# Optimization experiments

Measured on AMD Instinct MI355X. Metric: run time of the kernel, lower is better.

Reference implementation:

```python
import jax, jax.numpy as jnp
import numpy as np

EPS = 1e-5
NUM_MEM_TOKENS = 16
SEGMENT_SIZE = 512


def dpfp(x):
    # DPFP feature map (Schlag et al.), nu=1: doubles the last dim, all-nonnegative.
    x2 = jnp.concatenate([jax.nn.relu(x), jax.nn.relu(-x)], axis=-1)
    return x2 * jnp.roll(x2, 1, axis=-1)


def setup_inputs() -> dict:
    key = jax.random.key(0)
    ks = jax.random.split(key, 7)
    B, S, D, DM = 4, 4224, 1024, 64  # S = n_seg * (segment_size + num_mem_tokens) = 8*528
    scale = 0.02
    return {
        "hidden_states": jax.random.normal(ks[0], (B, S, D), jnp.float32),
        "model_output": jax.random.normal(ks[1], (B, S, D), jnp.float32),
        "W_mq": jax.random.normal(ks[2], (D, DM), jnp.float32) * scale,
        "W_mk": jax.random.normal(ks[3], (D, DM), jnp.float32) * scale,
        "W_mv": jax.random.normal(ks[4], (D, D), jnp.float32) * scale,
        "W_mb": jax.random.normal(ks[5], (D, D), jnp.float32) * scale,
        "b_mb": jnp.zeros((D,), jnp.float32),
    }


def reference(hidden_states, model_output, W_mq, W_mk, W_mv, W_mb, b_mb):
    B, S, D = hidden_states.shape
    L = SEGMENT_SIZE + NUM_MEM_TOKENS
    n_seg = S // L
    d_key = 2 * W_mq.shape[1]  # dpfp doubles feature dim

    # [n_seg, B, L, D]
    h = hidden_states.reshape(B, n_seg, L, D).transpose(1, 0, 2, 3)
    m = model_output.reshape(B, n_seg, L, D).transpose(1, 0, 2, 3)

    def step(carry, seg):
        W_mem, z = carry  # [B, d_key, D], [B, d_key]
        hid, mo = seg     # [B, L, D] each
        # --- associate: linear-attention read of compressive memory ---
        q = dpfp(hid @ W_mq)                                   # [B, L, d_key]
        num = jnp.einsum('blk,bkd->bld', q, W_mem)             # [B, L, D]
        den = jnp.einsum('blk,bk->bl', q, z)[..., None] + EPS
        assoc = num / den
        # --- delta-rule memory update from memory tokens of segment output ---
        mem = (assoc + mo)[:, -NUM_MEM_TOKENS:]                # [B, M, D]
        k = dpfp(mem @ W_mk)                                   # [B, M, d_key]
        v = mem @ W_mv                                         # [B, M, D]
        gate = jax.nn.sigmoid(mem @ W_mb + b_mb)               # [B, M, D]
        prev = jnp.einsum('bmk,bkd->bmd', k, W_mem) / (
            jnp.einsum('bmk,bk->bm', k, z)[..., None] + EPS)   # correction (old value)
        new_info = gate * (v - prev)
        W_mem = W_mem + jnp.einsum('bmk,bmd->bkd', k, new_info)
        z = z + k.sum(axis=1)
        return (W_mem, z), assoc

    W0 = jnp.zeros((B, d_key, D), hidden_states.dtype)
    z0 = jnp.zeros((B, d_key), hidden_states.dtype)
    _, assocs = jax.lax.scan(step, (W0, z0), (h, m))           # [n_seg, B, L, D]
    association = jnp.tanh(assocs.transpose(1, 0, 2, 3).reshape(B, S, D))
    return model_output + association
```

## Files before the change

kernel.cpp:

```cpp
#include <hip/hip_runtime.h>
#include <hip/hip_bf16.h>

#define EPS 1e-5f

typedef short s8v __attribute__((ext_vector_type(8)));
typedef float f4v __attribute__((ext_vector_type(4)));

__device__ __forceinline__ unsigned short f2bf(float f) {
  unsigned u = __builtin_bit_cast(unsigned, f);
  u = u + 0x7FFFu + ((u >> 16) & 1u);
  return (unsigned short)(u >> 16);
}
__device__ __forceinline__ float bf2f(unsigned short h) {
  unsigned u = ((unsigned)h) << 16;
  return __builtin_bit_cast(float, u);
}
__device__ __forceinline__ float fast_tanh(float x) {
  float e = __expf(2.0f * x);
  return 1.0f - 2.0f / (e + 1.0f);
}
__device__ __forceinline__ float fast_sigmoid(float x) {
  return 1.0f / (1.0f + __expf(-x));
}
__device__ __forceinline__ float frcp(float x) { return __builtin_amdgcn_rcpf(x); }

__global__ __launch_bounds__(256) void transpose_kernel(
    const float* __restrict__ W_mq, const float* __restrict__ W_mk,
    const float* __restrict__ W_mv, const float* __restrict__ W_mb,
    unsigned short* __restrict__ W_mqT, unsigned short* __restrict__ W_mkT,
    unsigned short* __restrict__ W_mvT, unsigned short* __restrict__ W_mbT) {
  __shared__ float tile[32][33];
  int bid = blockIdx.x;
  const float* src; unsigned short* dst; int N, t0;
  if (bid < 64)        { src = W_mq; dst = W_mqT; N = 64;   t0 = bid; }
  else if (bid < 128)  { src = W_mk; dst = W_mkT; N = 64;   t0 = bid - 64; }
  else if (bid < 1152) { src = W_mv; dst = W_mvT; N = 1024; t0 = bid - 128; }
  else                 { src = W_mb; dst = W_mbT; N = 1024; t0 = bid - 1152; }
  const int K = 1024;
  int tk = t0 & 31, tn = t0 >> 5;
  int k0 = tk * 32, n0 = tn * 32;
  int t = threadIdx.x;
  int cr = t >> 5, cc = t & 31;
#pragma unroll
  for (int u = 0; u < 4; u++) {
    int row = cr + u * 8;
    tile[row][cc] = src[(size_t)(k0 + row) * N + n0 + cc];
  }
  __syncthreads();
#pragma unroll
  for (int u = 0; u < 4; u++) {
    int nl = cr + u * 8;
    dst[(size_t)(n0 + nl) * K + k0 + cc] = f2bf(tile[cc][nl]);
  }
}

union QLdsU { float y[16 * 64]; unsigned short kq[16 * 128]; };

__device__ void q_tile_pair(const float* __restrict__ HS,
                            const unsigned short* __restrict__ W_mqT,
                            unsigned short* __restrict__ Q, int tile,
                            char* qsmem) {
  QLdsU* lds = (QLdsU*)qsmem;
  int t = threadIdx.x & 127, wv = t >> 6, lane = t & 63, m = lane & 15, q = lane >> 4;
  int r0 = tile * 16;
  const float* ap = HS + (size_t)(r0 + m) * 1024 + wv * 512 + q * 8;
  const unsigned short* bp = W_mqT + (size_t)m * 1024 + wv * 512 + q * 8;
  f4v acc[4] = {f4v{0,0,0,0}, f4v{0,0,0,0}, f4v{0,0,0,0}, f4v{0,0,0,0}};
#pragma unroll 4
  for (int ks = 0; ks < 16; ks++) {
    int k0 = ks * 32;
    f4v h0 = *(const f4v*)(ap + k0);
    f4v h1 = *(const f4v*)(ap + k0 + 4);
    s8v a;
    a[0] = (short)f2bf(h0[0]); a[1] = (short)f2bf(h0[1]);
    a[2] = (short)f2bf(h0[2]); a[3] = (short)f2bf(h0[3]);
    a[4] = (short)f2bf(h1[0]); a[5] = (short)f2bf(h1[1]);
    a[6] = (short)f2bf(h1[2]); a[7] = (short)f2bf(h1[3]);
#pragma unroll
    for (int nf = 0; nf < 4; nf++) {
      s8v b = *(const s8v*)(bp + nf * 16384 + k0);
      acc[nf] = __builtin_amdgcn_mfma_f32_16x16x32_bf16(a, b, acc[nf], 0, 0, 0);
    }
  }
  if (wv == 1) {
#pragma unroll
    for (int nf = 0; nf < 4; nf++)
#pragma unroll
      for (int i = 0; i < 4; i++)
        lds->y[(nf * 4 + i) * 64 + lane] = acc[nf][i];
  }
  __syncthreads();
  if (wv == 0) {
#pragma unroll
    for (int nf = 0; nf < 4; nf++)
#pragma unroll
      for (int i = 0; i < 4; i++)
        acc[nf][i] += lds->y[(nf * 4 + i) * 64 + lane];
    int srcl = (lane & 48) | ((m + 15) & 15);
#pragma unroll
    for (int i = 0; i < 4; i++) {
      float yp[4];
#pragma unroll
      for (int nf = 0; nf < 4; nf++) yp[nf] = __shfl(acc[nf][i], srcl);
      int r = q * 4 + i;
#pragma unroll
      for (int nf = 0; nf < 4; nf++) {
        float yv = acc[nf][i];
        float py = (m != 0) ? yp[nf] : (nf > 0 ? yp[nf - 1] : yp[3]);
        bool wrap = (m == 0 && nf == 0);
        float x2lo = wrap ? fmaxf(-py, 0.f) : fmaxf(py, 0.f);
        float x2hi = wrap ? fmaxf(py, 0.f) : fmaxf(-py, 0.f);
        lds->kq[r * 128 + nf * 16 + m]      = f2bf(fmaxf(yv, 0.f) * x2lo);
        lds->kq[r * 128 + 64 + nf * 16 + m] = f2bf(fmaxf(-yv, 0.f) * x2hi);
      }
    }
  }
  __syncthreads();
  {
    int row = t >> 3, ch = t & 7;
    unsigned short* qp = Q + (size_t)(r0 + row) * 128 + ch * 16;
    *(s8v*)(qp)     = *(const s8v*)&lds->kq[row * 128 + ch * 16];
    *(s8v*)(qp + 8) = *(const s8v*)&lds->kq[row * 128 + ch * 16 + 8];
  }
}

__device__ void scan_role(
    const float* __restrict__ HS, const unsigned short* __restrict__ W_mqT,
    const unsigned short* __restrict__ Qb, const unsigned short* __restrict__ W_mkT,
    const unsigned short* __restrict__ W_mvT, const unsigned short* __restrict__ W_mbT,
    const float* __restrict__ b_mb, const float* __restrict__ MO,
    float* __restrict__ OUT, unsigned short* __restrict__ hist,
    float* __restrict__ zh, unsigned short* __restrict__ mem_bf,
    int* bar, int* qflags, char* smem) {
  float* Wf           = (float*)smem;
  unsigned short* Wbf = (unsigned short*)(smem + 32768);
  float* y_lds        = (float*)(smem + 49664);
  float* k_f          = (float*)(smem + 53760);
  unsigned short* k_bf= (unsigned short*)(smem + 61952);
  float* kden_l       = (float*)(smem + 66304);
  float* ni_lds       = (float*)(smem + 66368);
  float* z_l          = (float*)(smem + 70528);

  int t = threadIdx.x, wv = t >> 6, lane = t & 63, m = lane & 15, q = lane >> 4;
  int ct = blockIdx.x & 15, b = blockIdx.x >> 4;
  int col = ct * 64 + wv * 16 + m;

  if (blockIdx.x < 16) {
    int pair = t >> 7;
    int sp = blockIdx.x * 2 + pair;
    int tile = (sp >> 3) * 264 + (sp & 7) * 33 + 32;
    q_tile_pair(HS, W_mqT, (unsigned short*)Qb, tile, smem + pair * 4096);
    __syncthreads();
    if (t == 0) { __threadfence(); atomicAdd(qflags, 2); }
  }

  for (int i = t; i < 128 * 64; i += 256) Wf[i] = 0.f;
  for (int i = t; i < 64 * 132; i += 256) Wbf[i] = 0;
  if (t < 128) z_l[t] = 0.f;
  float bmb = b_mb[col];
  if (t == 0) {
    while (__hip_atomic_load(qflags, __ATOMIC_RELAXED, __HIP_MEMORY_SCOPE_AGENT) < 32)
      __builtin_amdgcn_s_sleep(1);
    __threadfence();
  }
  __syncthreads();

  s8v aq[4]; float mo_pf[4];
  {
    const unsigned short* qp = Qb + ((size_t)b * 4224 + 512 + m) * 128;
#pragma unroll
    for (int ks = 0; ks < 4; ks++) aq[ks] = *(const s8v*)(qp + ks * 32 + q * 8);
    const float* mop = MO + ((size_t)b * 4224 + 512 + q * 4) * 1024 + col;
#pragma unroll
    for (int i = 0; i < 4; i++) mo_pf[i] = mop[(size_t)i * 1024];
  }

  for (int s = 0; s < 8; s++) {
    {
      float dp = 0.f;
#pragma unroll
      for (int ks = 0; ks < 4; ks++)
#pragma unroll
        for (int j = 0; j < 8; j++)
          dp += bf2f((unsigned short)aq[ks][j]) * z_l[ks * 32 + q * 8 + j];
      dp += __shfl_xor(dp, 16);
      dp += __shfl_xor(dp, 32);
      dp += EPS;
      f4v acc = {0, 0, 0, 0};
#pragma unroll
      for (int ks = 0; ks < 4; ks++) {
        s8v bv = *(const s8v*)&Wbf[(wv * 16 + m) * 132 + ks * 32 + q * 8];
        acc = __builtin_amdgcn_mfma_f32_16x16x32_bf16(aq[ks], bv, acc, 0, 0, 0);
      }
      unsigned short* mb = mem_bf + (s & 1) * 65536 + b * 16384;
      size_t grow = (size_t)b * 4224 + s * 528 + 512;
#pragma unroll
      for (int i = 0; i < 4; i++) {
        float rden = frcp(__shfl(dp, q * 4 + i));
        float assoc = acc[i] * rden;
        float mov = mo_pf[i];
        OUT[(grow + q * 4 + i) * 1024 + col] = mov + fast_tanh(assoc);
        mb[(q * 4 + i) * 1024 + col] = f2bf(assoc + mov);
      }
    }
    __syncthreads();
    if (t == 0) {
      __threadfence();
      atomicAdd(bar + s * 4 + b, 1);
      while (__hip_atomic_load(bar + s * 4 + b, __ATOMIC_RELAXED,
                               __HIP_MEMORY_SCOPE_AGENT) < 16)
        __builtin_amdgcn_s_sleep(1);
      __threadfence();
    }
    __syncthreads();
    f4v accv = {0,0,0,0}, accg = {0,0,0,0};
    {
      const unsigned short* avp = mem_bf + (s & 1) * 65536 + b * 16384 + m * 1024 + q * 8;
      const unsigned short* bkp = W_mkT + (size_t)(wv * 16 + m) * 1024 + q * 8;
      const unsigned short* bvp = W_mvT + (size_t)col * 1024 + q * 8;
      const unsigned short* bgp = W_mbT + (size_t)col * 1024 + q * 8;
      f4v acy = {0, 0, 0, 0};
#pragma unroll 4
      for (int ks = 0; ks < 32; ks++) {
        s8v av = *(const s8v*)(avp + ks * 32);
        s8v bk = *(const s8v*)(bkp + ks * 32);
        s8v bv = *(const s8v*)(bvp + ks * 32);
        s8v bg = *(const s8v*)(bgp + ks * 32);
        acy  = __builtin_amdgcn_mfma_f32_16x16x32_bf16(av, bk, acy, 0, 0, 0);
        accv = __builtin_amdgcn_mfma_f32_16x16x32_bf16(av, bv, accv, 0, 0, 0);
        accg = __builtin_amdgcn_mfma_f32_16x16x32_bf16(av, bg, accg, 0, 0, 0);
      }
#pragma unroll
      for (int i = 0; i < 4; i++) y_lds[(q * 4 + i) * 64 + wv * 16 + m] = acy[i];
    }
    __syncthreads();
    {
      int r = t >> 4, jg = t & 15;
      const float* yr = &y_lds[r * 64];
      float pd = 0.f;
#pragma unroll
      for (int u = 0; u < 8; u++) {
        int jj = jg * 8 + u, jm = (jj + 127) & 127;
        float yj = (jj < 64) ? yr[jj] : -yr[jj - 64];
        float ym = (jm < 64) ? yr[jm] : -yr[jm - 64];
        float kv = fmaxf(yj, 0.f) * fmaxf(ym, 0.f);
        k_f[r * 128 + jj] = kv;
        k_bf[r * 136 + jj] = f2bf(kv);
        pd += kv * z_l[jj];
      }
      pd += __shfl_xor(pd, 1);
      pd += __shfl_xor(pd, 2);
      pd += __shfl_xor(pd, 4);
      pd += __shfl_xor(pd, 8);
      if (jg == 0) kden_l[r] = pd + EPS;
    }
    __syncthreads();
    {
      f4v accp = {0, 0, 0, 0};
#pragma unroll
      for (int ks = 0; ks < 4; ks++) {
        s8v ak = *(const s8v*)&k_bf[m * 136 + ks * 32 + q * 8];
        s8v bm = *(const s8v*)&Wbf[(wv * 16 + m) * 132 + ks * 32 + q * 8];
        accp = __builtin_amdgcn_mfma_f32_16x16x32_bf16(ak, bm, accp, 0, 0, 0);
      }
#pragma unroll
      for (int i = 0; i < 4; i++) {
        int r = q * 4 + i;
        float prev = accp[i] * frcp(kden_l[r]);
        float g = fast_sigmoid(accg[i] + bmb);
        ni_lds[r * 65 + wv * 16 + m] = g * (accv[i] - prev);
      }
      if (t < 128) {
        float ssum = 0.f;
#pragma unroll
        for (int r = 0; r < 16; r++) ssum += k_f[r * 128 + t];
        z_l[t] += ssum;
        if (s < 7) zh[(s + 1) * 512 + b * 128 + t] = z_l[t];
      }
    }
    __syncthreads();
    {
      int cl = t & 63, kg = t >> 6;
      float niv[16];
#pragma unroll
      for (int mm = 0; mm < 16; mm++) niv[mm] = ni_lds[mm * 65 + cl];
      float delta[32];
#pragma unroll
      for (int jj = 0; jj < 32; jj++) delta[jj] = 0.f;
#pragma unroll
      for (int mm = 0; mm < 16; mm++) {
        const float* kb = &k_f[mm * 128 + kg * 32];
        float nv = niv[mm];
#pragma unroll
        for (int ch = 0; ch < 8; ch++) {
          f4v kv4 = *(const f4v*)(kb + ch * 4);
#pragma unroll
          for (int jj = 0; jj < 4; jj++) delta[ch * 4 + jj] += kv4[jj] * nv;
        }
      }
      unsigned short* hdst = hist + (size_t)(s + 1) * 524288 +
                             ((size_t)b * 1024 + ct * 64 + cl) * 128 + kg * 32;
#pragma unroll
      for (int c8 = 0; c8 < 4; c8++) {
        s8v pk;
#pragma unroll
        for (int u = 0; u < 8; u++) {
          int kk = kg * 32 + c8 * 8 + u;
          float nv = Wf[kk * 64 + cl] + delta[c8 * 8 + u];
          Wf[kk * 64 + cl] = nv;
          pk[u] = (short)f2bf(nv);
        }
        *(s8v*)&Wbf[cl * 132 + kg * 32 + c8 * 8] = pk;
        if (s < 7) *(s8v*)(hdst + c8 * 8) = pk;
      }
      if (s < 7) {
        const unsigned short* qp = Qb + ((size_t)b * 4224 + (s + 1) * 528 + 512 + m) * 128;
#pragma unroll
        for (int ks = 0; ks < 4; ks++) aq[ks] = *(const s8v*)(qp + ks * 32 + q * 8);
        const float* mop = MO + ((size_t)b * 4224 + (s + 1) * 528 + 512 + q * 4) * 1024 + col;
#pragma unroll
        for (int i = 0; i < 4; i++) mo_pf[i] = mop[(size_t)i * 1024];
      }
    }
    __syncthreads();
  }
}

__device__ void worker_role(
    const float* __restrict__ HS, const unsigned short* __restrict__ W_mqT,
    unsigned short* __restrict__ Qb, const unsigned short* __restrict__ hist,
    const float* __restrict__ zh, const float* __restrict__ MO,
    float* __restrict__ OUT, int* bar, int* qflags, char* smem) {
  int w = (int)blockIdx.x - 64;
  int t = threadIdx.x;
  int pair = t >> 7;
  int np = 0;
  for (int p = w; p < 512; p += 192) {
    int rr = 2 * p + pair;
    int tile = (rr >> 8) * 264 + ((rr & 255) >> 5) * 33 + (rr & 31);
    q_tile_pair(HS, W_mqT, Qb, tile, smem + pair * 4096);
    np++;
    __syncthreads();
  }
  if (t == 0) { __threadfence(); atomicAdd(qflags + 1, np); }
  for (int idx = w; idx < 512; idx += 192) {
    int b = idx & 3, ct = (idx >> 2) & 15, rt4 = idx >> 6;
    int r = t >> 2, cchunk = (t & 3) * 16;
    size_t rbase = ((size_t)b * 4224 + (size_t)rt4 * 64 + r) * 1024 + ct * 64 + cchunk;
#pragma unroll
    for (int u = 0; u < 4; u++)
      *(f4v*)(OUT + rbase + u * 4) = *(const f4v*)(MO + rbase + u * 4);
  }
  if (t == 0) {
    while (__hip_atomic_load(qflags + 1, __ATOMIC_RELAXED, __HIP_MEMORY_SCOPE_AGENT) < 512)
      __builtin_amdgcn_s_sleep(1);
    __threadfence();
  }
  __syncthreads();
  int wv = t >> 6, lane = t & 63, m = lane & 15, q = lane >> 4;
  float* as_l = (float*)smem;
  for (int idx = 512 + w; idx < 4096; idx += 192) {
    int seg = idx >> 9, inner = idx & 511;
    int b = inner & 3, ct = (inner >> 2) & 15, rt4 = inner >> 6;
    if (t == 0) {
      while (__hip_atomic_load(bar + seg * 4 + b, __ATOMIC_RELAXED,
                               __HIP_MEMORY_SCOPE_AGENT) < 16)
        __builtin_amdgcn_s_sleep(2);
      __threadfence();
    }
    __syncthreads();
    const unsigned short* Wm = hist + (size_t)seg * 524288 + ((size_t)b * 1024 + ct * 64) * 128;
    const float* zp = zh + seg * 512 + b * 128;
    size_t grow = (size_t)b * 4224 + (size_t)seg * 528 + rt4 * 64 + wv * 16;
    const unsigned short* qp = Qb + (grow + m) * 128;
    s8v a[4];
    float dp = 0.f;
#pragma unroll
    for (int ks = 0; ks < 4; ks++) {
      a[ks] = *(const s8v*)(qp + ks * 32 + q * 8);
      f4v z0 = *(const f4v*)(zp + ks * 32 + q * 8);
      f4v z1 = *(const f4v*)(zp + ks * 32 + q * 8 + 4);
#pragma unroll
      for (int j = 0; j < 4; j++) dp += bf2f((unsigned short)a[ks][j]) * z0[j];
#pragma unroll
      for (int j = 0; j < 4; j++) dp += bf2f((unsigned short)a[ks][j + 4]) * z1[j];
    }
    dp += __shfl_xor(dp, 16);
    dp += __shfl_xor(dp, 32);
    dp += EPS;
    f4v acc[4] = {f4v{0,0,0,0}, f4v{0,0,0,0}, f4v{0,0,0,0}, f4v{0,0,0,0}};
#pragma unroll
    for (int ks = 0; ks < 4; ks++) {
#pragma unroll
      for (int nf = 0; nf < 4; nf++) {
        s8v bv = *(const s8v*)(Wm + (size_t)(nf * 16 + m) * 128 + ks * 32 + q * 8);
        acc[nf] = __builtin_amdgcn_mfma_f32_16x16x32_bf16(a[ks], bv, acc[nf], 0, 0, 0);
      }
    }
#pragma unroll
    for (int i = 0; i < 4; i++) {
      float rden = frcp(__shfl(dp, q * 4 + i));
#pragma unroll
      for (int nf = 0; nf < 4; nf++)
        as_l[(wv * 16 + q * 4 + i) * 65 + nf * 16 + m] = acc[nf][i] * rden;
    }
    __syncthreads();
    {
      int r = t >> 2, cchunk = (t & 3) * 16;
      size_t rbase = (grow - wv * 16 + r) * 1024 + ct * 64 + cchunk;
      const float* ar = &as_l[r * 65 + cchunk];
#pragma unroll
      for (int u = 0; u < 4; u++) {
        f4v mo = *(const f4v*)(MO + rbase + u * 4);
        f4v o;
#pragma unroll
        for (int j = 0; j < 4; j++) o[j] = mo[j] + fast_tanh(ar[u * 4 + j]);
        *(f4v*)(OUT + rbase + u * 4) = o;
      }
    }
    __syncthreads();
  }
}

__global__ __launch_bounds__(256, 1) void fused_kernel(
    const float* __restrict__ HS, const unsigned short* __restrict__ W_mqT,
    const unsigned short* __restrict__ W_mkT, const unsigned short* __restrict__ W_mvT,
    const unsigned short* __restrict__ W_mbT, const float* __restrict__ b_mb,
    const float* __restrict__ MO, float* __restrict__ OUT,
    unsigned short* __restrict__ Qb, unsigned short* __restrict__ hist,
    float* __restrict__ zh, unsigned short* __restrict__ mem_bf,
    int* bar, int* qflags) {
  __shared__ __align__(16) char smem[71040];
  if (blockIdx.x < 64) {
    scan_role(HS, W_mqT, Qb, W_mkT, W_mvT, W_mbT, b_mb, MO, OUT,
              hist, zh, mem_bf, bar, qflags, smem);
  } else {
    worker_role(HS, W_mqT, Qb, hist, zh, MO, OUT, bar, qflags, smem);
  }
}

extern "C" void kernel_launch(void* const* d_in, const int* in_sizes, int n_in,
                              void* d_out, int out_size, void* d_ws, size_t ws_size,
                              hipStream_t stream) {
  const float* HS  = (const float*)d_in[0];
  const float* MO  = (const float*)d_in[1];
  const float* W_mq = (const float*)d_in[2];
  const float* W_mk = (const float*)d_in[3];
  const float* W_mv = (const float*)d_in[4];
  const float* W_mb = (const float*)d_in[5];
  const float* b_mb = (const float*)d_in[6];
  float* OUT = (float*)d_out;

  char* wsb = (char*)d_ws;
  unsigned short* hist   = (unsigned short*)(wsb + 0);
  float*          zh     = (float*)(wsb + 8388608);
  unsigned short* Qb     = (unsigned short*)(wsb + 8404992);
  unsigned short* W_mqT  = (unsigned short*)(wsb + 12730368);
  unsigned short* W_mkT  = (unsigned short*)(wsb + 12861440);
  unsigned short* W_mvT  = (unsigned short*)(wsb + 12992512);
  unsigned short* W_mbT  = (unsigned short*)(wsb + 15089664);
  unsigned short* mem_bf = (unsigned short*)(wsb + 17186816);
  int*            bar    = (int*)(wsb + 17448960);
  int*            qflags = (int*)(wsb + 0);

  (void)hipMemsetAsync(wsb, 0, 256, stream);
  (void)hipMemsetAsync(bar, 0, 128, stream);
  transpose_kernel<<<2176, 256, 0, stream>>>(W_mq, W_mk, W_mv, W_mb,
                                             W_mqT, W_mkT, W_mvT, W_mbT);
  fused_kernel<<<256, 256, 0, stream>>>(HS, W_mqT, W_mkT, W_mvT, W_mbT, b_mb,
                                        MO, OUT, Qb, hist, zh, mem_bf, bar, qflags);
}
```

Before: 527.9 us.

## Use atomic work queue for bulk tiles, double grid, pad barrier counters

Bulk output tiles are now pulled from a global atomic work queue instead of a static stride, and scan blocks join the bulk loop once their sequential scan finishes. The grid doubles to 512 blocks with launch bounds allowing 2 blocks per CU, and per-segment barrier counters are padded to separate cache lines with longer sleep intervals. The goal is better load balance and more latency hiding across the bulk phase. In exchange, scan blocks may now share CUs with worker blocks and slow the serial critical path, and the spin barriers rely on all 512 blocks being co-resident.

New measurement: 787.7 us. +49.2%, slower.

```diff
diff --git a/kernel.cpp b/kernel.cpp
--- a/kernel.cpp
+++ b/kernel.cpp
@@ -124,6 +124,80 @@
   }
 }
 
+__device__ void bulk_loop(const unsigned short* __restrict__ Qb,
+                          const unsigned short* __restrict__ hist,
+                          const float* __restrict__ zh,
+                          const float* __restrict__ MO, float* __restrict__ OUT,
+                          int* bar, int* wq, char* smem) {
+  int t = threadIdx.x, wv = t >> 6, lane = t & 63, m = lane & 15, q = lane >> 4;
+  float* as_l = (float*)smem;
+  int* sidx = (int*)(smem + 16640);
+  for (;;) {
+    if (t == 0) sidx[0] = atomicAdd(wq, 1);
+    __syncthreads();
+    int idx = sidx[0] + 512;
+    if (idx >= 4096) break;
+    int seg = idx >> 9, inner = idx & 511;
+    int b = inner & 3, ct = (inner >> 2) & 15, rt4 = inner >> 6;
+    if (t == 0) {
+      while (__hip_atomic_load(bar + (seg * 4 + b) * 16, __ATOMIC_RELAXED,
+                               __HIP_MEMORY_SCOPE_AGENT) < 16)
+        __builtin_amdgcn_s_sleep(8);
+      __threadfence();
+    }
+    __syncthreads();
+    const unsigned short* Wm = hist + (size_t)seg * 524288 + ((size_t)b * 1024 + ct * 64) * 128;
+    const float* zp = zh + seg * 512 + b * 128;
+    size_t grow = (size_t)b * 4224 + (size_t)seg * 528 + rt4 * 64 + wv * 16;
+    const unsigned short* qp = Qb + (grow + m) * 128;
+    s8v a[4];
+    float dp = 0.f;
+#pragma unroll
+    for (int ks = 0; ks < 4; ks++) {
+      a[ks] = *(const s8v*)(qp + ks * 32 + q * 8);
+      f4v z0 = *(const f4v*)(zp + ks * 32 + q * 8);
+      f4v z1 = *(const f4v*)(zp + ks * 32 + q * 8 + 4);
+#pragma unroll
+      for (int j = 0; j < 4; j++) dp += bf2f((unsigned short)a[ks][j]) * z0[j];
+#pragma unroll
+      for (int j = 0; j < 4; j++) dp += bf2f((unsigned short)a[ks][j + 4]) * z1[j];
+    }
+    dp += __shfl_xor(dp, 16);
+    dp += __shfl_xor(dp, 32);
+    dp += EPS;
+    f4v acc[4] = {f4v{0,0,0,0}, f4v{0,0,0,0}, f4v{0,0,0,0}, f4v{0,0,0,0}};
+#pragma unroll
+    for (int ks = 0; ks < 4; ks++) {
+#pragma unroll
+      for (int nf = 0; nf < 4; nf++) {
+        s8v bv = *(const s8v*)(Wm + (size_t)(nf * 16 + m) * 128 + ks * 32 + q * 8);
+        acc[nf] = __builtin_amdgcn_mfma_f32_16x16x32_bf16(a[ks], bv, acc[nf], 0, 0, 0);
+      }
+    }
+#pragma unroll
+    for (int i = 0; i < 4; i++) {
+      float rden = frcp(__shfl(dp, q * 4 + i));
+#pragma unroll
+      for (int nf = 0; nf < 4; nf++)
+        as_l[(wv * 16 + q * 4 + i) * 65 + nf * 16 + m] = acc[nf][i] * rden;
+    }
+    __syncthreads();
+    {
+      int r = t >> 2, cchunk = (t & 3) * 16;
+      size_t rbase = (grow - wv * 16 + r) * 1024 + ct * 64 + cchunk;
+      const float* ar = &as_l[r * 65 + cchunk];
+#pragma unroll
+      for (int u = 0; u < 4; u++) {
+        f4v mo = *(const f4v*)(MO + rbase + u * 4);
+        f4v o;
+#pragma unroll
+        for (int j = 0; j < 4; j++) o[j] = mo[j] + fast_tanh(ar[u * 4 + j]);
+        *(f4v*)(OUT + rbase + u * 4) = o;
+      }
+    }
+  }
+}
+
 __device__ void scan_role(
     const float* __restrict__ HS, const unsigned short* __restrict__ W_mqT,
     const unsigned short* __restrict__ Qb, const unsigned short* __restrict__ W_mkT,
@@ -131,7 +205,7 @@
     const float* __restrict__ b_mb, const float* __restrict__ MO,
     float* __restrict__ OUT, unsigned short* __restrict__ hist,
     float* __restrict__ zh, unsigned short* __restrict__ mem_bf,
-    int* bar, int* qflags, char* smem) {
+    int* bar, int* qflags, int* wq, char* smem) {
   float* Wf           = (float*)smem;
   unsigned short* Wbf = (unsigned short*)(smem + 32768);
   float* y_lds        = (float*)(smem + 49664);
@@ -206,8 +280,8 @@
     __syncthreads();
     if (t == 0) {
       __threadfence();
-      atomicAdd(bar + s * 4 + b, 1);
-      while (__hip_atomic_load(bar + s * 4 + b, __ATOMIC_RELAXED,
+      atomicAdd(bar + (s * 4 + b) * 16, 1);
+      while (__hip_atomic_load(bar + (s * 4 + b) * 16, __ATOMIC_RELAXED,
                                __HIP_MEMORY_SCOPE_AGENT) < 16)
         __builtin_amdgcn_s_sleep(1);
       __threadfence();
@@ -324,18 +398,27 @@
     }
     __syncthreads();
   }
+
+  if (t == 0) {
+    while (__hip_atomic_load(qflags + 1, __ATOMIC_RELAXED, __HIP_MEMORY_SCOPE_AGENT) < 512)
+      __builtin_amdgcn_s_sleep(8);
+    __threadfence();
+  }
+  __syncthreads();
+  bulk_loop(Qb, hist, zh, MO, OUT, bar, wq, smem);
 }
 
 __device__ void worker_role(
     const float* __restrict__ HS, const unsigned short* __restrict__ W_mqT,
     unsigned short* __restrict__ Qb, const unsigned short* __restrict__ hist,
     const float* __restrict__ zh, const float* __restrict__ MO,
-    float* __restrict__ OUT, int* bar, int* qflags, char* smem) {
+    float* __restrict__ OUT, int* bar, int* qflags, int* wq, char* smem) {
+  int nw = (int)gridDim.x - 64;
   int w = (int)blockIdx.x - 64;
   int t = threadIdx.x;
   int pair = t >> 7;
   int np = 0;
-  for (int p = w; p < 512; p += 192) {
+  for (int p = w; p < 512; p += nw) {
     int rr = 2 * p + pair;
     int tile = (rr >> 8) * 264 + ((rr & 255) >> 5) * 33 + (rr & 31);
     q_tile_pair(HS, W_mqT, Qb, tile, smem + pair * 4096);
@@ -343,7 +426,7 @@
     __syncthreads();
   }
   if (t == 0) { __threadfence(); atomicAdd(qflags + 1, np); }
-  for (int idx = w; idx < 512; idx += 192) {
+  for (int idx = w; idx < 512; idx += nw) {
     int b = idx & 3, ct = (idx >> 2) & 15, rt4 = idx >> 6;
     int r = t >> 2, cchunk = (t & 3) * 16;
     size_t rbase = ((size_t)b * 4224 + (size_t)rt4 * 64 + r) * 1024 + ct * 64 + cchunk;
@@ -353,89 +436,27 @@
   }
   if (t == 0) {
     while (__hip_atomic_load(qflags + 1, __ATOMIC_RELAXED, __HIP_MEMORY_SCOPE_AGENT) < 512)
-      __builtin_amdgcn_s_sleep(1);
+      __builtin_amdgcn_s_sleep(8);
     __threadfence();
   }
   __syncthreads();
-  int wv = t >> 6, lane = t & 63, m = lane & 15, q = lane >> 4;
-  float* as_l = (float*)smem;
-  for (int idx = 512 + w; idx < 4096; idx += 192) {
-    int seg = idx >> 9, inner = idx & 511;
-    int b = inner & 3, ct = (inner >> 2) & 15, rt4 = inner >> 6;
-    if (t == 0) {
-      while (__hip_atomic_load(bar + seg * 4 + b, __ATOMIC_RELAXED,
-                               __HIP_MEMORY_SCOPE_AGENT) < 16)
-        __builtin_amdgcn_s_sleep(2);
-      __threadfence();
-    }
-    __syncthreads();
-    const unsigned short* Wm = hist + (size_t)seg * 524288 + ((size_t)b * 1024 + ct * 64) * 128;
-    const float* zp = zh + seg * 512 + b * 128;
-    size_t grow = (size_t)b * 4224 + (size_t)seg * 528 + rt4 * 64 + wv * 16;
-    const unsigned short* qp = Qb + (grow + m) * 128;
-    s8v a[4];
-    float dp = 0.f;
-#pragma unroll
-    for (int ks = 0; ks < 4; ks++) {
-      a[ks] = *(const s8v*)(qp + ks * 32 + q * 8);
-      f4v z0 = *(const f4v*)(zp + ks * 32 + q * 8);
-      f4v z1 = *(const f4v*)(zp + ks * 32 + q * 8 + 4);
-#pragma unroll
-      for (int j = 0; j < 4; j++) dp += bf2f((unsigned short)a[ks][j]) * z0[j];
-#pragma unroll
-      for (int j = 0; j < 4; j++) dp += bf2f((unsigned short)a[ks][j + 4]) * z1[j];
-    }
-    dp += __shfl_xor(dp, 16);
-    dp += __shfl_xor(dp, 32);
-    dp += EPS;
-    f4v acc[4] = {f4v{0,0,0,0}, f4v{0,0,0,0}, f4v{0,0,0,0}, f4v{0,0,0,0}};
-#pragma unroll
-    for (int ks = 0; ks < 4; ks++) {
-#pragma unroll
-      for (int nf = 0; nf < 4; nf++) {
-        s8v bv = *(const s8v*)(Wm + (size_t)(nf * 16 + m) * 128 + ks * 32 + q * 8);
-        acc[nf] = __builtin_amdgcn_mfma_f32_16x16x32_bf16(a[ks], bv, acc[nf], 0, 0, 0);
-      }
-    }
-#pragma unroll
-    for (int i = 0; i < 4; i++) {
-      float rden = frcp(__shfl(dp, q * 4 + i));
-#pragma unroll
-      for (int nf = 0; nf < 4; nf++)
-        as_l[(wv * 16 + q * 4 + i) * 65 + nf * 16 + m] = acc[nf][i] * rden;
-    }
-    __syncthreads();
-    {
-      int r = t >> 2, cchunk = (t & 3) * 16;
-      size_t rbase = (grow - wv * 16 + r) * 1024 + ct * 64 + cchunk;
-      const float* ar = &as_l[r * 65 + cchunk];
-#pragma unroll
-      for (int u = 0; u < 4; u++) {
-        f4v mo = *(const f4v*)(MO + rbase + u * 4);
-        f4v o;
-#pragma unroll
-        for (int j = 0; j < 4; j++) o[j] = mo[j] + fast_tanh(ar[u * 4 + j]);
-        *(f4v*)(OUT + rbase + u * 4) = o;
-      }
-    }
-    __syncthreads();
-  }
-}
-
-__global__ __launch_bounds__(256, 1) void fused_kernel(
+  bulk_loop(Qb, hist, zh, MO, OUT, bar, wq, smem);
+}
+
+__global__ __launch_bounds__(256, 2) void fused_kernel(
     const float* __restrict__ HS, const unsigned short* __restrict__ W_mqT,
     const unsigned short* __restrict__ W_mkT, const unsigned short* __restrict__ W_mvT,
     const unsigned short* __restrict__ W_mbT, const float* __restrict__ b_mb,
     const float* __restrict__ MO, float* __restrict__ OUT,
     unsigned short* __restrict__ Qb, unsigned short* __restrict__ hist,
     float* __restrict__ zh, unsigned short* __restrict__ mem_bf,
-    int* bar, int* qflags) {
+    int* bar, int* qflags, int* wq) {
   __shared__ __align__(16) char smem[71040];
   if (blockIdx.x < 64) {
     scan_role(HS, W_mqT, Qb, W_mkT, W_mvT, W_mbT, b_mb, MO, OUT,
-              hist, zh, mem_bf, bar, qflags, smem);
+              hist, zh, mem_bf, bar, qflags, wq, smem);
   } else {
-    worker_role(HS, W_mqT, Qb, hist, zh, MO, OUT, bar, qflags, smem);
+    worker_role(HS, W_mqT, Qb, hist, zh, MO, OUT, bar, qflags, wq, smem);
   }
 }
 
@@ -460,13 +481,13 @@
   unsigned short* W_mvT  = (unsigned short*)(wsb + 12992512);
   unsigned short* W_mbT  = (unsigned short*)(wsb + 15089664);
   unsigned short* mem_bf = (unsigned short*)(wsb + 17186816);
-  int*            bar    = (int*)(wsb + 17448960);
   int*            qflags = (int*)(wsb + 0);
-
-  (void)hipMemsetAsync(wsb, 0, 256, stream);
-  (void)hipMemsetAsync(bar, 0, 128, stream);
+  int*            wq     = (int*)(wsb + 512);
+  int*            bar    = (int*)(wsb + 1024);
+
+  (void)hipMemsetAsync(wsb, 0, 4096, stream);
   transpose_kernel<<<2176, 256, 0, stream>>>(W_mq, W_mk, W_mv, W_mb,
                                              W_mqT, W_mkT, W_mvT, W_mbT);
-  fused_kernel<<<256, 256, 0, stream>>>(HS, W_mqT, W_mkT, W_mvT, W_mbT, b_mb,
-                                        MO, OUT, Qb, hist, zh, mem_bf, bar, qflags);
-}
+  fused_kernel<<<512, 256, 0, stream>>>(HS, W_mqT, W_mkT, W_mvT, W_mbT, b_mb,
+                                        MO, OUT, Qb, hist, zh, mem_bf, bar, qflags, wq);
+}
```
